# Kernel tuning notes

Measured on AMD Instinct MI355X. Metric: run time of the kernel, lower is better.

## Reference

```python
import jax, jax.numpy as jnp
import numpy as np

N = 50000
E = 800000
H = 8
DH = 32  # hidden 256 / heads 8


def gat_layer(h, src, dst, W, a_src, a_dst, b):
    # h: [N, 256] -> per-head projected features [N, H, DH]
    hp = (h @ W).reshape(N, H, DH)
    # per-node attention logits for src/dst roles: [N, H]
    s_src = jnp.einsum('nhd,hd->nh', hp, a_src)
    s_dst = jnp.einsum('nhd,hd->nh', hp, a_dst)
    e = jax.nn.leaky_relu(s_src[src] + s_dst[dst], negative_slope=0.2)  # [Et, H]
    # segment softmax over incoming edges of each dst node
    m = jax.ops.segment_max(e, dst, num_segments=N)  # [N, H]
    ex = jnp.exp(e - m[dst])
    denom = jax.ops.segment_sum(ex, dst, num_segments=N)  # [N, H] (>0: self-loops)
    alpha = ex / denom[dst]  # [Et, H]
    out = jax.ops.segment_sum(alpha[:, :, None] * hp[src], dst, num_segments=N)
    return out.reshape(N, H * DH) + b


def han_forward(x, edges, proj_W, proj_b, gat_W, gat_asrc, gat_adst, gat_b,
                sem_W1, sem_b1, sem_W2, cls_W1, cls_b1, cls_W2, cls_b2):
    h0 = x @ proj_W + proj_b  # [N, 256]
    loop = jnp.arange(N, dtype=edges.dtype)
    embs = []
    for p in range(edges.shape[0]):  # 3 meta-paths (fixed, small)
        src = jnp.concatenate([edges[p, 0], loop])  # add self-loops (PyG default)
        dst = jnp.concatenate([edges[p, 1], loop])
        h = h0
        for l in range(2):  # 2 GAT layers per meta-path
            h = gat_layer(h, src, dst, gat_W[p, l], gat_asrc[p, l], gat_adst[p, l], gat_b[p, l])
            h = jax.nn.elu(h)  # dropout: eval-mode no-op
        embs.append(h)
    emb = jnp.stack(embs, axis=1)  # [N, P, 256]
    scores = (jnp.tanh(emb @ sem_W1 + sem_b1) @ sem_W2).squeeze(-1)  # [N, P]
    w = jax.nn.softmax(scores, axis=1)
    z = jnp.sum(emb * w[:, :, None], axis=1)  # [N, 256]
    hcls = jax.nn.relu(z @ cls_W1 + cls_b1)
    logits = hcls @ cls_W2 + cls_b2  # [N, 2]
    return logits


def setup_inputs() -> dict:
    key = jax.random.key(0)
    ks = jax.random.split(key, 16)
    s = 0.05
    return {
        'x': jax.random.normal(ks[0], (N, 128), jnp.float32),
        'edges': jax.random.randint(ks[1], (3, 2, E), 0, N, dtype=jnp.int32),
        'proj_W': jax.random.normal(ks[2], (128, 256), jnp.float32) * s,
        'proj_b': jnp.zeros((256,), jnp.float32),
        'gat_W': jax.random.normal(ks[3], (3, 2, 256, 256), jnp.float32) * s,
        'gat_asrc': jax.random.normal(ks[4], (3, 2, H, DH), jnp.float32) * s,
        'gat_adst': jax.random.normal(ks[5], (3, 2, H, DH), jnp.float32) * s,
        'gat_b': jnp.zeros((3, 2, 256), jnp.float32),
        'sem_W1': jax.random.normal(ks[6], (256, 128), jnp.float32) * s,
        'sem_b1': jnp.zeros((128,), jnp.float32),
        'sem_W2': jax.random.normal(ks[7], (128, 1), jnp.float32) * s,
        'cls_W1': jax.random.normal(ks[8], (256, 128), jnp.float32) * s,
        'cls_b1': jnp.zeros((128,), jnp.float32),
        'cls_W2': jax.random.normal(ks[9], (128, 2), jnp.float32) * s,
        'cls_b2': jnp.zeros((2,), jnp.float32),
    }


def reference(x, edges, proj_W, proj_b, gat_W, gat_asrc, gat_adst, gat_b,
              sem_W1, sem_b1, sem_W2, cls_W1, cls_b1, cls_W2, cls_b2):
    return han_forward(x, edges, proj_W, proj_b, gat_W, gat_asrc, gat_adst, gat_b,
                       sem_W1, sem_b1, sem_W2, cls_W1, cls_b1, cls_W2, cls_b2)
```

## Files before the change

### kernel.cpp

```cpp
#include <hip/hip_runtime.h>
#include <hip/hip_fp16.h>
#include <math.h>

#define N_NODES 50000
#define N_EDG   800000
#define NH      8
#define DH      32
#define HID     256
#define MAXD    64
#define EPB     4096
#define PROJ_FB 88
#define PROJ_EB (176*EPB)
#define G3_FB   69
#define AGGB    12500

typedef __attribute__((ext_vector_type(8))) short bf16x8;
typedef __attribute__((ext_vector_type(4))) float f32x4;

#define GLL16(src, dst) __builtin_amdgcn_global_load_lds(                  \
    (const __attribute__((address_space(1))) void*)(const void*)(src),     \
    (__attribute__((address_space(3))) void*)(dst), 16, 0, 0)

__device__ __forceinline__ unsigned short f2bf(float x) {
    unsigned u = __float_as_uint(x);
    u += 0x7FFF + ((u >> 16) & 1);
    return (unsigned short)(u >> 16);
}
__device__ __forceinline__ float bf2f(unsigned short h) {
    return __uint_as_float(((unsigned)h) << 16);
}
__device__ __forceinline__ float fastrcp(float x) {
    float r;
    asm("v_rcp_f32 %0, %1" : "=v"(r) : "v"(x));
    return r;
}
__device__ __forceinline__ void split8(const float4& a, const float4& b,
                                       uint4& hi, uint4& lo) {
    float v[8] = {a.x,a.y,a.z,a.w,b.x,b.y,b.z,b.w};
    unsigned short h[8], l[8];
    #pragma unroll
    for (int i = 0; i < 8; ++i) { h[i] = f2bf(v[i]); l[i] = f2bf(v[i] - bf2f(h[i])); }
    hi = make_uint4(h[0]|((unsigned)h[1]<<16), h[2]|((unsigned)h[3]<<16),
                    h[4]|((unsigned)h[5]<<16), h[6]|((unsigned)h[7]<<16));
    lo = make_uint4(l[0]|((unsigned)l[1]<<16), l[2]|((unsigned)l[3]<<16),
                    l[4]|((unsigned)l[5]<<16), l[6]|((unsigned)l[7]<<16));
}
__device__ __forceinline__ void h8_to_pair(uint4 r, uint4& hi, uint4& lo) {
    const __half2* hp = (const __half2*)&r;
    unsigned short h[8], l[8];
    #pragma unroll
    for (int i = 0; i < 4; ++i) {
        float2 f = __half22float2(hp[i]);
        h[2*i]   = f2bf(f.x); l[2*i]   = f2bf(f.x - bf2f(h[2*i]));
        h[2*i+1] = f2bf(f.y); l[2*i+1] = f2bf(f.y - bf2f(h[2*i+1]));
    }
    hi = make_uint4(h[0]|((unsigned)h[1]<<16), h[2]|((unsigned)h[3]<<16),
                    h[4]|((unsigned)h[5]<<16), h[6]|((unsigned)h[7]<<16));
    lo = make_uint4(l[0]|((unsigned)l[1]<<16), l[2]|((unsigned)l[3]<<16),
                    l[4]|((unsigned)l[5]<<16), l[6]|((unsigned)l[7]<<16));
}

__device__ __forceinline__ void fmix2(float& alo, float& ahi, unsigned rv, float w) {
    asm("v_fma_mix_f32 %0, %1, %2, %0 op_sel:[0,0,0] op_sel_hi:[1,0,0]"
        : "+v"(alo) : "v"(rv), "v"(w));
    asm("v_fma_mix_f32 %0, %1, %2, %0 op_sel:[1,0,0] op_sel_hi:[1,0,0]"
        : "+v"(ahi) : "v"(rv), "v"(w));
}

__device__ __forceinline__ void fill_edges(const int* __restrict__ edges,
                                           int* __restrict__ cnt3,
                                           unsigned short* __restrict__ slots3,
                                           int fb, int ebase) {
    const int base = ebase + fb * EPB + (int)threadIdx.x;
    #pragma unroll 1
    for (int t = 0; t < 4; ++t) {
        int dd[4], ss[4];
        #pragma unroll
        for (int j = 0; j < 4; ++j) {
            int e = base + (t * 4 + j) * 256;
            if (e < 3 * N_EDG) {
                int p = e / N_EDG, i = e - p * N_EDG;
                const int* src = edges + (size_t)p * 2 * N_EDG;
                int s = src[i], d = src[N_EDG + i];
                ss[j] = min(max(s, 0), N_NODES - 1);
                dd[j] = p * N_NODES + min(max(d, 0), N_NODES - 1);
            } else { ss[j] = -1; dd[j] = 0; }
        }
        int pos[4];
        #pragma unroll
        for (int j = 0; j < 4; ++j)
            if (ss[j] >= 0) pos[j] = atomicAdd(&cnt3[dd[j]], 1);
        #pragma unroll
        for (int j = 0; j < 4; ++j)
            if (ss[j] >= 0 && pos[j] < MAXD)
                slots3[(size_t)dd[j] * MAXD + pos[j]] = (unsigned short)ss[j];
    }
}

__device__ __forceinline__ void agg_worker(
    int fb, int p, int l,
    const int* __restrict__ cnt3, const unsigned short* __restrict__ slots3,
    const float* __restrict__ ssrc3, const float* __restrict__ sdst3,
    const __half* __restrict__ hp3, const float* __restrict__ gatB,
    __half* __restrict__ emb16) {
    const int wid  = fb * 4 + ((int)threadIdx.x >> 6);
    const int lane = threadIdx.x & 63;
    if (wid >= N_NODES) return;
    const int n = wid;
    const unsigned short* srcs = slots3 + ((size_t)p * N_NODES + n) * MAXD;
    const float* s_src = ssrc3 + p * N_NODES * NH;
    const float* s_dst = sdst3 + p * N_NODES * NH;
    const __half* hp = hp3 + (size_t)p * N_NODES * HID;
    const float* bias = gatB + (2*p + l) * HID;
    const int deg = min(cnt3[p * N_NODES + n], MAXD);

    const int sub = lane & 31, eo = lane >> 5;
    const int h2  = sub >> 2;
    const float sd2 = s_dst[n*NH + h2];
    const uint4* hp4 = (const uint4*)hp;
    float dn = 0.f;
    float a0=0.f,a1=0.f,a2=0.f,a3=0.f,a4=0.f,a5=0.f,a6=0.f,a7=0.f;

    int i = eo;
    for (; i + 6 < deg; i += 8) {
        const int s0 = srcs[i];
        const int s1 = srcs[i + 2];
        const int s2 = srcs[i + 4];
        const int s3 = srcs[i + 6];
        const float x0 = s_src[s0*NH + h2];
        const float x1 = s_src[s1*NH + h2];
        const float x2 = s_src[s2*NH + h2];
        const float x3 = s_src[s3*NH + h2];
        const uint4 r0 = hp4[s0*32 + sub];
        const uint4 r1 = hp4[s1*32 + sub];
        const uint4 r2 = hp4[s2*32 + sub];
        const uint4 r3 = hp4[s3*32 + sub];
        float e0 = x0 + sd2; e0 = e0 > 0.f ? e0 : 0.2f * e0;
        float e1 = x1 + sd2; e1 = e1 > 0.f ? e1 : 0.2f * e1;
        float e2 = x2 + sd2; e2 = e2 > 0.f ? e2 : 0.2f * e2;
        float e3 = x3 + sd2; e3 = e3 > 0.f ? e3 : 0.2f * e3;
        const float w0 = __expf(e0), w1 = __expf(e1);
        const float w2 = __expf(e2), w3 = __expf(e3);
        dn += w0; dn += w1; dn += w2; dn += w3;
        fmix2(a0, a1, r0.x, w0); fmix2(a2, a3, r0.y, w0);
        fmix2(a4, a5, r0.z, w0); fmix2(a6, a7, r0.w, w0);
        fmix2(a0, a1, r1.x, w1); fmix2(a2, a3, r1.y, w1);
        fmix2(a4, a5, r1.z, w1); fmix2(a6, a7, r1.w, w1);
        fmix2(a0, a1, r2.x, w2); fmix2(a2, a3, r2.y, w2);
        fmix2(a4, a5, r2.z, w2); fmix2(a6, a7, r2.w, w2);
        fmix2(a0, a1, r3.x, w3); fmix2(a2, a3, r3.y, w3);
        fmix2(a4, a5, r3.z, w3); fmix2(a6, a7, r3.w, w3);
    }
    for (; i + 2 < deg; i += 4) {
        const int s0 = srcs[i];
        const int s1 = srcs[i + 2];
        const float x0 = s_src[s0*NH + h2];
        const float x1 = s_src[s1*NH + h2];
        const uint4 r0 = hp4[s0*32 + sub];
        const uint4 r1 = hp4[s1*32 + sub];
        float e0 = x0 + sd2; e0 = e0 > 0.f ? e0 : 0.2f * e0;
        float e1 = x1 + sd2; e1 = e1 > 0.f ? e1 : 0.2f * e1;
        const float w0 = __expf(e0), w1 = __expf(e1);
        dn += w0; dn += w1;
        fmix2(a0, a1, r0.x, w0); fmix2(a2, a3, r0.y, w0);
        fmix2(a4, a5, r0.z, w0); fmix2(a6, a7, r0.w, w0);
        fmix2(a0, a1, r1.x, w1); fmix2(a2, a3, r1.y, w1);
        fmix2(a4, a5, r1.z, w1); fmix2(a6, a7, r1.w, w1);
    }
    if (i < deg) {
        const int s0 = srcs[i];
        const float x0 = s_src[s0*NH + h2];
        const uint4 r0 = hp4[s0*32 + sub];
        float e0 = x0 + sd2; e0 = e0 > 0.f ? e0 : 0.2f * e0;
        const float w0 = __expf(e0);
        dn += w0;
        fmix2(a0, a1, r0.x, w0); fmix2(a2, a3, r0.y, w0);
        fmix2(a4, a5, r0.z, w0); fmix2(a6, a7, r0.w, w0);
    }
    dn += __shfl_xor(dn, 32);
    a0 += __shfl_xor(a0, 32); a1 += __shfl_xor(a1, 32);
    a2 += __shfl_xor(a2, 32); a3 += __shfl_xor(a3, 32);
    a4 += __shfl_xor(a4, 32); a5 += __shfl_xor(a5, 32);
    a6 += __shfl_xor(a6, 32); a7 += __shfl_xor(a7, 32);
    if (lane < 32) {
        float evs = s_src[n*NH + h2] + sd2;
        evs = evs > 0.f ? evs : 0.2f * evs;
        float ws = __expf(evs);
        dn += ws;
        const uint4 rs = hp4[n*32 + sub];
        fmix2(a0, a1, rs.x, ws); fmix2(a2, a3, rs.y, ws);
        fmix2(a4, a5, rs.z, ws); fmix2(a6, a7, rs.w, ws);

        float rdn = fastrcp(dn);
        float v[8] = {a0,a1,a2,a3,a4,a5,a6,a7};
        const float4 b0 = *(const float4*)&bias[sub*8];
        const float4 b1 = *(const float4*)&bias[sub*8 + 4];
        v[0]=v[0]*rdn+b0.x; v[1]=v[1]*rdn+b0.y; v[2]=v[2]*rdn+b0.z; v[3]=v[3]*rdn+b0.w;
        v[4]=v[4]*rdn+b1.x; v[5]=v[5]*rdn+b1.y; v[6]=v[6]*rdn+b1.z; v[7]=v[7]*rdn+b1.w;
        unsigned short hh[8];
        #pragma unroll
        for (int k = 0; k < 8; ++k) {
            float e = v[k] > 0.f ? v[k] : (__expf(v[k]) - 1.f);
            hh[k] = __half_as_ushort(__float2half(e));
        }
        size_t o = ((size_t)p * N_NODES + n) * HID + sub * 8;
        *(uint4*)&emb16[o] = make_uint4(hh[0]|((unsigned)hh[1]<<16), hh[2]|((unsigned)hh[3]<<16),
                                        hh[4]|((unsigned)hh[5]<<16), hh[6]|((unsigned)hh[7]<<16));
    }
}

__global__ __launch_bounds__(256)
void agg3y_k(const int* __restrict__ cnt3, const unsigned short* __restrict__ slots3,
             const float* __restrict__ ssrc3, const float* __restrict__ sdst3,
             const __half* __restrict__ hp3, const float* __restrict__ gatB,
             int l, __half* __restrict__ emb16) {
    agg_worker(blockIdx.x, blockIdx.y, l, cnt3, slots3, ssrc3, sdst3, hp3, gatB, emb16);
}

template<int NC, int ACT, int OUTMODE, int AMODE, int FILL>
__global__ __launch_bounds__(256)
void mfma_gemm_k(const float* __restrict__ A32p, const __half* __restrict__ A16p,
                 int lda,
                 const unsigned short* __restrict__ WThi,
                 const unsigned short* __restrict__ WTlo,
                 const float* __restrict__ bias,
                 float* __restrict__ C, __half* __restrict__ Ch,
                 int ldc, int M, int K,
                 const int* __restrict__ edges, int* __restrict__ cnt3,
                 unsigned short* __restrict__ slots3,
                 const float* __restrict__ w4z,
                 int aplanez, int cplanez) {
    __shared__ unsigned short sAh[128*32], sAl[128*32], sBh[128*32], sBl[128*32];
    const int gxk = (M + 127) >> 7;
    if constexpr (FILL) {
        if ((int)blockIdx.x >= gxk) {
            fill_edges(edges, cnt3, slots3,
                       ((int)blockIdx.x - gxk) + PROJ_FB * (int)blockIdx.y, 0);
            return;
        }
    }
    if (A16p) A16p += (size_t)blockIdx.z * aplanez;
    if (C)    C    += (size_t)blockIdx.z * cplanez;
    const int tid  = threadIdx.x;
    const int lane = tid & 63;
    const int w    = tid >> 6;
    const int wr   = w >> 1, wc = w & 1;
    const int r0   = blockIdx.x * 128;
    const int c0   = blockIdx.y * 128;
    const int l15  = lane & 15, q = lane >> 4;

    const int cl8   = (((lane & 3) ^ ((lane >> 4) & 3)) << 3);
    const int lrow  = w*32 + (lane >> 2);
    const int gbrow0 = c0 + lrow, gbrow1 = c0 + lrow + 16;
    const int lbase = w * 1024;

    const int srow = tid >> 2, slot = tid & 3;
    const int arow0 = min(r0 + srow,      M - 1);
    const int arow1 = min(r0 + srow + 64, M - 1);
    const size_t ga0 = (size_t)arow0 * lda + slot * 8;
    const size_t ga1 = (size_t)arow1 * lda + slot * 8;
    const int lda0 = srow*32 + ((slot ^ ((srow >> 2) & 3)) << 3);
    const int lda1 = lda0 + 64*32;

    float4 w0r, w1r;
    if constexpr (AMODE == 3) {
        w0r = *(const float4*)&w4z[arow0 * 4];
        w1r = *(const float4*)&w4z[arow1 * 4];
    }

    f32x4 acc[4][4];
    #pragma unroll
    for (int i = 0; i < 4; ++i)
        #pragma unroll
        for (int j = 0; j < 4; ++j) acc[i][j] = (f32x4){0.f, 0.f, 0.f, 0.f};

    const int swzF = (l15 >> 2) & 3;
    const int qs   = ((q ^ swzF) << 3);

    const int nsteps = K >> 5;
    for (int s = 0; s < nsteps; ++s) {
        const int kc = s << 5;
        __syncthreads();
        GLL16(&WThi[(size_t)gbrow0*K + kc + cl8], &sBh[lbase]);
        GLL16(&WThi[(size_t)gbrow1*K + kc + cl8], &sBh[lbase + 512]);
        GLL16(&WTlo[(size_t)gbrow0*K + kc + cl8], &sBl[lbase]);
        GLL16(&WTlo[(size_t)gbrow1*K + kc + cl8], &sBl[lbase + 512]);
        uint4 h0, l0, h1, l1;
        if constexpr (AMODE == 0) {
            float4 f0a = *(const float4*)&A32p[ga0 + kc];
            float4 f0b = *(const float4*)&A32p[ga0 + kc + 4];
            float4 f1a = *(const float4*)&A32p[ga1 + kc];
            float4 f1b = *(const float4*)&A32p[ga1 + kc + 4];
            split8(f0a, f0b, h0, l0);
            split8(f1a, f1b, h1, l1);
        } else if constexpr (AMODE == 1) {
            uint4 r0v = *(const uint4*)&A16p[ga0 + kc];
            uint4 r1v = *(const uint4*)&A16p[ga1 + kc];
            h8_to_pair(r0v, h0, l0);
            h8_to_pair(r1v, h1, l1);
        } else {
            const int off = kc + slot * 8;
            #pragma unroll
            for (int rr = 0; rr < 2; ++rr) {
                const int row = rr ? arow1 : arow0;
                const float4 wv = rr ? w1r : w0r;
                const __half2* e0 = (const __half2*)&A16p[(size_t)row * HID + off];
                const __half2* e1 = (const __half2*)&A16p[((size_t)N_NODES + row) * HID + off];
                const __half2* e2 = (const __half2*)&A16p[((size_t)2*N_NODES + row) * HID + off];
                float vv[8];
                #pragma unroll
                for (int j2 = 0; j2 < 4; ++j2) {
                    float2 fa = __half22float2(e0[j2]);
                    float2 fb2 = __half22float2(e1[j2]);
                    float2 fc = __half22float2(e2[j2]);
                    vv[2*j2]   = wv.x*fa.x + wv.y*fb2.x + wv.z*fc.x;
                    vv[2*j2+1] = wv.x*fa.y + wv.y*fb2.y + wv.z*fc.y;
                }
                if (rr) split8(*(const float4*)&vv[0], *(const float4*)&vv[4], h1, l1);
                else    split8(*(const float4*)&vv[0], *(const float4*)&vv[4], h0, l0);
            }
        }
        *(uint4*)&sAh[lda0] = h0; *(uint4*)&sAl[lda0] = l0;
        *(uint4*)&sAh[lda1] = h1; *(uint4*)&sAl[lda1] = l1;
        __syncthreads();

        bf16x8 fAh[4], fAl[4];
        #pragma unroll
        for (int t = 0; t < 4; ++t) {
            int ra = (wr*64 + t*16 + l15) * 32 + qs;
            fAh[t] = *(const bf16x8*)&sAh[ra];
            fAl[t] = *(const bf16x8*)&sAl[ra];
        }
        #pragma unroll
        for (int nt = 0; nt < 4; ++nt) {
            int rb = (wc*64 + nt*16 + l15) * 32 + qs;
            bf16x8 fBh = *(const bf16x8*)&sBh[rb];
            bf16x8 fBl = *(const bf16x8*)&sBl[rb];
            #pragma unroll
            for (int mt = 0; mt < 4; ++mt) {
                acc[mt][nt] = __builtin_amdgcn_mfma_f32_16x16x32_bf16(fAh[mt], fBh, acc[mt][nt], 0, 0, 0);
                acc[mt][nt] = __builtin_amdgcn_mfma_f32_16x16x32_bf16(fAh[mt], fBl, acc[mt][nt], 0, 0, 0);
                acc[mt][nt] = __builtin_amdgcn_mfma_f32_16x16x32_bf16(fAl[mt], fBh, acc[mt][nt], 0, 0, 0);
            }
        }
    }
    #pragma unroll
    for (int mt = 0; mt < 4; ++mt)
        #pragma unroll
        for (int nt = 0; nt < 4; ++nt) {
            int col = c0 + wc*64 + nt*16 + l15;
            float bb = bias ? bias[col] : 0.f;
            #pragma unroll
            for (int r = 0; r < 4; ++r) {
                int grow = r0 + wr*64 + mt*16 + q*4 + r;
                if (grow < M) {
                    float v = acc[mt][nt][r] + bb;
                    if (ACT == 1) {
                        float t = __expf(2.f * v);
                        v = 1.f - 2.f * fastrcp(1.f + t);
                    } else if (ACT == 2) v = fmaxf(v, 0.f);
                    size_t o = (size_t)grow * ldc + col;
                    if (OUTMODE == 2) Ch[o] = __float2half(v);
                    else              C[o] = v;
                }
            }
        }
}

template<int FILL>
__global__ __launch_bounds__(256)
void mfma_gemm3_k(const __half* __restrict__ A16p, int aoffz, int lda,
                  const unsigned short* __restrict__ WT, int l,
                  __half* __restrict__ hp3, int M,
                  const int* __restrict__ edges, int* __restrict__ cnt3,
                  unsigned short* __restrict__ slots3) {
    __shared__ unsigned short sAh[128*32], sAl[128*32], sBh[128*32], sBl[128*32];
    const int gx = (M + 127) >> 7;
    if constexpr (FILL) {
        if ((int)blockIdx.x >= gx) {
            fill_edges(edges, cnt3, slots3,
                       ((int)blockIdx.x - gx) + G3_FB * ((int)blockIdx.y + 2 * (int)blockIdx.z),
                       PROJ_EB);
            return;
        }
    }
    const int p = blockIdx.z;
    const __half* Ap = A16p + (size_t)p * aoffz;
    const unsigned short* WThi = WT + (size_t)(2*p + l) * 131072;
    const unsigned short* WTlo = WThi + 65536;
    __half* Ch = hp3 + (size_t)p * N_NODES * HID;
    const int K = HID;

    const int tid  = threadIdx.x;
    const int lane = tid & 63;
    const int w    = tid >> 6;
    const int wr   = w >> 1, wc = w & 1;
    const int r0   = blockIdx.x * 128;
    const int c0   = blockIdx.y * 128;
    const int l15  = lane & 15, q = lane >> 4;

    const int cl8   = (((lane & 3) ^ ((lane >> 4) & 3)) << 3);
    const int lrow  = w*32 + (lane >> 2);
    const int gbrow0 = c0 + lrow, gbrow1 = c0 + lrow + 16;
    const int lbase = w * 1024;

    const int srow = tid >> 2, slot = tid & 3;
    const size_t ga0 = (size_t)min(r0 + srow,      M - 1) * lda + slot * 8;
    const size_t ga1 = (size_t)min(r0 + srow + 64, M - 1) * lda + slot * 8;
    const int lda0 = srow*32 + ((slot ^ ((srow >> 2) & 3)) << 3);
    const int lda1 = lda0 + 64*32;

    f32x4 acc[4][4];
    #pragma unroll
    for (int i = 0; i < 4; ++i)
        #pragma unroll
        for (int j = 0; j < 4; ++j) acc[i][j] = (f32x4){0.f, 0.f, 0.f, 0.f};

    const int swzF = (l15 >> 2) & 3;
    const int qs   = ((q ^ swzF) << 3);

    for (int s = 0; s < 8; ++s) {
        const int kc = s << 5;
        __syncthreads();
        GLL16(&WThi[(size_t)gbrow0*K + kc + cl8], &sBh[lbase]);
        GLL16(&WThi[(size_t)gbrow1*K + kc + cl8], &sBh[lbase + 512]);
        GLL16(&WTlo[(size_t)gbrow0*K + kc + cl8], &sBl[lbase]);
        GLL16(&WTlo[(size_t)gbrow1*K + kc + cl8], &sBl[lbase + 512]);
        uint4 r0v = *(const uint4*)&Ap[ga0 + kc];
        uint4 r1v = *(const uint4*)&Ap[ga1 + kc];
        uint4 h0, l0, h1, l1;
        h8_to_pair(r0v, h0, l0);
        h8_to_pair(r1v, h1, l1);
        *(uint4*)&sAh[lda0] = h0; *(uint4*)&sAl[lda0] = l0;
        *(uint4*)&sAh[lda1] = h1; *(uint4*)&sAl[lda1] = l1;
        __syncthreads();

        bf16x8 fAh[4], fAl[4];
        #pragma unroll
        for (int t = 0; t < 4; ++t) {
            int ra = (wr*64 + t*16 + l15) * 32 + qs;
            fAh[t] = *(const bf16x8*)&sAh[ra];
            fAl[t] = *(const bf16x8*)&sAl[ra];
        }
        #pragma unroll
        for (int nt = 0; nt < 4; ++nt) {
            int rb = (wc*64 + nt*16 + l15) * 32 + qs;
            bf16x8 fBh = *(const bf16x8*)&sBh[rb];
            bf16x8 fBl = *(const bf16x8*)&sBl[rb];
            #pragma unroll
            for (int mt = 0; mt < 4; ++mt) {
                acc[mt][nt] = __builtin_amdgcn_mfma_f32_16x16x32_bf16(fAh[mt], fBh, acc[mt][nt], 0, 0, 0);
                acc[mt][nt] = __builtin_amdgcn_mfma_f32_16x16x32_bf16(fAh[mt], fBl, acc[mt][nt], 0, 0, 0);
                acc[mt][nt] = __builtin_amdgcn_mfma_f32_16x16x32_bf16(fAl[mt], fBh, acc[mt][nt], 0, 0, 0);
            }
        }
    }
    #pragma unroll
    for (int mt = 0; mt < 4; ++mt)
        #pragma unroll
        for (int nt = 0; nt < 4; ++nt) {
            int col = c0 + wc*64 + nt*16 + l15;
            #pragma unroll
            for (int r = 0; r < 4; ++r) {
                int grow = r0 + wr*64 + mt*16 + q*4 + r;
                if (grow < M)
                    Ch[(size_t)grow * HID + col] = __float2half(acc[mt][nt][r]);
            }
        }
}

__global__ __launch_bounds__(256)
void cvtWall_k(const float* __restrict__ gatW, const float* __restrict__ projW,
               const float* __restrict__ semW1, const float* __restrict__ clsW1,
               unsigned short* __restrict__ WT) {
    int y = blockIdx.y;
    const float* W; int K, N;
    if (y < 6)       { W = gatW + (size_t)y * 65536; K = 256; N = 256; }
    else if (y == 6) { W = projW; K = 128; N = 256; }
    else if (y == 7) { W = semW1; K = 256; N = 128; }
    else             { W = clsW1; K = 256; N = 128; }
    int idx = blockIdx.x * 256 + threadIdx.x;
    if (idx >= K * N) return;
    unsigned short* hi = WT + (size_t)y * 131072;
    unsigned short* lo = hi + 65536;
    int k = idx / N, n = idx - k * N;
    float v = W[idx];
    unsigned short h = f2bf(v);
    hi[n * K + k] = h;
    lo[n * K + k] = f2bf(v - bf2f(h));
}

__global__ __launch_bounds__(256)
void attn_scores3_k(const __half* __restrict__ hp3,
                    const float* __restrict__ gatAs, const float* __restrict__ gatAd,
                    int l, int pbase, float* __restrict__ ssrc3, float* __restrict__ sdst3) {
    int p = pbase + blockIdx.y;
    int gid = blockIdx.x * 256 + threadIdx.x;
    if (gid >= N_NODES * NH) return;
    int h = gid & 7;
    const __half2* hv = (const __half2*)(hp3 + (size_t)p * N_NODES * HID + (size_t)gid * DH);
    const float* a = gatAs + (2*p + l) * HID + h * DH;
    const float* d = gatAd + (2*p + l) * HID + h * DH;
    float ss = 0.f, sd = 0.f;
    #pragma unroll
    for (int j = 0; j < 8; ++j) {
        float4 av = ((const float4*)a)[j], dv = ((const float4*)d)[j];
        float2 f0 = __half22float2(hv[2*j]);
        float2 f1 = __half22float2(hv[2*j + 1]);
        ss += f0.x*av.x + f0.y*av.y + f1.x*av.z + f1.y*av.w;
        sd += f0.x*dv.x + f0.y*dv.y + f1.x*dv.z + f1.y*dv.w;
    }
    ssrc3[p * N_NODES * NH + gid] = ss;
    sdst3[p * N_NODES * NH + gid] = sd;
}

__global__ __launch_bounds__(256)
void zero_k(int* p, int n) { int i = blockIdx.x*256 + threadIdx.x; if (i < n) p[i] = 0; }

__global__ __launch_bounds__(256)
void score_w_k(const float* __restrict__ tb, const float* __restrict__ W2,
               float* __restrict__ w4) {
    int wid  = (blockIdx.x * blockDim.x + threadIdx.x) >> 6;
    int lane = threadIdx.x & 63;
    if (wid >= N_NODES) return;
    const int n = wid;
    float sc[3];
    #pragma unroll
    for (int p = 0; p < 3; ++p) {
        const float* tr = tb + (size_t)p * N_NODES * 128 + (size_t)n * 128;
        float part = tr[lane] * W2[lane] + tr[64 + lane] * W2[64 + lane];
        #pragma unroll
        for (int o = 1; o < 64; o <<= 1) part += __shfl_xor(part, o);
        sc[p] = part;
    }
    float m  = fmaxf(sc[0], fmaxf(sc[1], sc[2]));
    float e0 = __expf(sc[0]-m), e1 = __expf(sc[1]-m), e2 = __expf(sc[2]-m);
    float rs = fastrcp(e0 + e1 + e2);
    if (lane == 0)
        *(float4*)&w4[(size_t)n * 4] = make_float4(e0*rs, e1*rs, e2*rs, 0.f);
}

__global__ __launch_bounds__(256)
void logits_k(const float* __restrict__ hcls, const float* __restrict__ W2,
              const float* __restrict__ b2, float* __restrict__ out) {
    int gid = blockIdx.x*256 + threadIdx.x;
    if (gid >= N_NODES * 2) return;
    int n = gid >> 1, o = gid & 1;
    const float* hr = hcls + (size_t)n * 128;
    float a = b2[o];
    #pragma unroll 4
    for (int j = 0; j < 128; ++j) a += hr[j] * W2[j*2 + o];
    out[gid] = a;
}

extern "C" void kernel_launch(void* const* d_in, const int* in_sizes, int n_in,
                              void* d_out, int out_size, void* d_ws, size_t ws_size,
                              hipStream_t stream) {
    (void)in_sizes; (void)n_in; (void)out_size; (void)ws_size;
    const float* x     = (const float*)d_in[0];
    const int*   edges = (const int*)  d_in[1];
    const float* projW = (const float*)d_in[2];
    const float* projb = (const float*)d_in[3];
    const float* gatW  = (const float*)d_in[4];
    const float* gatAs = (const float*)d_in[5];
    const float* gatAd = (const float*)d_in[6];
    const float* gatB  = (const float*)d_in[7];
    const float* semW1 = (const float*)d_in[8];
    const float* semb1 = (const float*)d_in[9];
    const float* semW2 = (const float*)d_in[10];
    const float* clsW1 = (const float*)d_in[11];
    const float* clsb1 = (const float*)d_in[12];
    const float* clsW2 = (const float*)d_in[13];
    const float* clsb2 = (const float*)d_in[14];
    float* out = (float*)d_out;

    char* base = (char*)d_ws;
    const size_t PLANE = (size_t)N_NODES * HID * 2;
    __half* hp3   = (__half*)(base);
    __half* emb16 = (__half*)(base + 3*PLANE);
    __half* h016  = (__half*)(base + 6*PLANE);
    char* small = base + 7*PLANE;
    float* ssrc3 = (float*)small;
    float* sdst3 = ssrc3 + 3*(size_t)N_NODES*NH;
    int*   cnt3  = (int*)(sdst3 + 3*(size_t)N_NODES*NH);
    unsigned short* WT = (unsigned short*)(cnt3 + 3*N_NODES);
    unsigned short* slots3 = WT + 9*131072;
    float* w4 = (float*)(slots3 + (size_t)3*N_NODES*MAXD);
    float* t0 = (float*)(base);
    float* hcls = (float*)(base + 6*PLANE);

    dim3 blk(256);
    const int gx = (N_NODES + 127) / 128;

    cvtWall_k<<<dim3(256, 9), blk, 0, stream>>>(gatW, projW, semW1, clsW1, WT);
    zero_k  <<<(3*N_NODES+255)/256, blk, 0, stream>>>(cnt3, 3*N_NODES);

    mfma_gemm_k<256,0,2,0,1><<<dim3(gx + PROJ_FB, 2), blk, 0, stream>>>(
        x, nullptr, 128, WT + 6*131072, WT + 6*131072 + 65536, projb,
        nullptr, h016, 256, N_NODES, 128, edges, cnt3, slots3, nullptr, 0, 0);

    mfma_gemm3_k<1><<<dim3(gx + G3_FB, 2, 3), blk, 0, stream>>>(
        h016, 0, HID, WT, 0, hp3, N_NODES, edges, cnt3, slots3);

    attn_scores3_k<<<dim3((N_NODES*NH+255)/256, 3), blk, 0, stream>>>(
        hp3, gatAs, gatAd, 0, 0, ssrc3, sdst3);

    agg3y_k<<<dim3(AGGB, 3), blk, 0, stream>>>(
        cnt3, slots3, ssrc3, sdst3, hp3, gatB, 0, emb16);

    mfma_gemm3_k<0><<<dim3(gx, 2, 3), blk, 0, stream>>>(
        emb16, (int)((size_t)N_NODES*HID), HID, WT, 1, hp3, N_NODES,
        nullptr, nullptr, nullptr);

    attn_scores3_k<<<dim3((N_NODES*NH+255)/256, 3), blk, 0, stream>>>(
        hp3, gatAs, gatAd, 1, 0, ssrc3, sdst3);

    agg3y_k<<<dim3(AGGB, 3), blk, 0, stream>>>(
        cnt3, slots3, ssrc3, sdst3, hp3, gatB, 1, emb16);

    mfma_gemm_k<128,1,0,1,0><<<dim3(gx, 1, 3), blk, 0, stream>>>(
        nullptr, emb16, 256, WT + 7*131072, WT + 7*131072 + 65536, semb1,
        t0, nullptr, 128, N_NODES, 256, nullptr, nullptr, nullptr, nullptr,
        (int)((size_t)N_NODES*HID), N_NODES*128);

    score_w_k<<<dim3(AGGB), blk, 0, stream>>>(t0, semW2, w4);

    mfma_gemm_k<128,2,0,3,0><<<dim3(gx, 1), blk, 0, stream>>>(
        nullptr, emb16, HID, WT + 8*131072, WT + 8*131072 + 65536, clsb1,
        hcls, nullptr, 128, N_NODES, 256, nullptr, nullptr, nullptr, w4, 0, 0);

    logits_k<<<(N_NODES*2+255)/256, blk, 0, stream>>>(hcls, clsW2, clsb2, out);
}
```

Baseline: 968.1 us.

## Fuse classifier output layer into cls GEMM epilogue and use packed bf16 convert

The final 128->2 logits projection moves into the epilogue of the classifier GEMM. Each row's two outputs are reduced across lanes with shuffles and across the two column-warps through shared memory, so the hcls intermediate is no longer written and re-read and the separate logits kernel launch goes away. In the same change, the bf16 hi/lo splitting helpers switch from manual rounding to the packed v_cvt_pk_bf16_f32 instruction, which cuts ALU work wherever operands are split. The new epilogue adds shuffles and a barrier to the GEMM tail.

```diff
diff --git a/kernel.cpp b/kernel.cpp
--- a/kernel.cpp
+++ b/kernel.cpp
@@ -29,6 +29,11 @@
 __device__ __forceinline__ float bf2f(unsigned short h) {
     return __uint_as_float(((unsigned)h) << 16);
 }
+__device__ __forceinline__ unsigned cvtpk_bf16(float a, float b) {
+    unsigned r;
+    asm("v_cvt_pk_bf16_f32 %0, %1, %2" : "=v"(r) : "v"(a), "v"(b));
+    return r;
+}
 __device__ __forceinline__ float fastrcp(float x) {
     float r;
     asm("v_rcp_f32 %0, %1" : "=v"(r) : "v"(x));
@@ -36,28 +41,31 @@
 }
 __device__ __forceinline__ void split8(const float4& a, const float4& b,
                                        uint4& hi, uint4& lo) {
-    float v[8] = {a.x,a.y,a.z,a.w,b.x,b.y,b.z,b.w};
-    unsigned short h[8], l[8];
-    #pragma unroll
-    for (int i = 0; i < 8; ++i) { h[i] = f2bf(v[i]); l[i] = f2bf(v[i] - bf2f(h[i])); }
-    hi = make_uint4(h[0]|((unsigned)h[1]<<16), h[2]|((unsigned)h[3]<<16),
-                    h[4]|((unsigned)h[5]<<16), h[6]|((unsigned)h[7]<<16));
-    lo = make_uint4(l[0]|((unsigned)l[1]<<16), l[2]|((unsigned)l[3]<<16),
-                    l[4]|((unsigned)l[5]<<16), l[6]|((unsigned)l[7]<<16));
+    float f[8] = {a.x,a.y,a.z,a.w,b.x,b.y,b.z,b.w};
+    unsigned hpk[4], lpk[4];
+    #pragma unroll
+    for (int i = 0; i < 4; ++i) {
+        hpk[i] = cvtpk_bf16(f[2*i], f[2*i+1]);
+        float hl = __uint_as_float(hpk[i] << 16);
+        float hh = __uint_as_float(hpk[i] & 0xffff0000u);
+        lpk[i] = cvtpk_bf16(f[2*i] - hl, f[2*i+1] - hh);
+    }
+    hi = make_uint4(hpk[0], hpk[1], hpk[2], hpk[3]);
+    lo = make_uint4(lpk[0], lpk[1], lpk[2], lpk[3]);
 }
 __device__ __forceinline__ void h8_to_pair(uint4 r, uint4& hi, uint4& lo) {
     const __half2* hp = (const __half2*)&r;
-    unsigned short h[8], l[8];
+    unsigned hpk[4], lpk[4];
     #pragma unroll
     for (int i = 0; i < 4; ++i) {
         float2 f = __half22float2(hp[i]);
-        h[2*i]   = f2bf(f.x); l[2*i]   = f2bf(f.x - bf2f(h[2*i]));
-        h[2*i+1] = f2bf(f.y); l[2*i+1] = f2bf(f.y - bf2f(h[2*i+1]));
-    }
-    hi = make_uint4(h[0]|((unsigned)h[1]<<16), h[2]|((unsigned)h[3]<<16),
-                    h[4]|((unsigned)h[5]<<16), h[6]|((unsigned)h[7]<<16));
-    lo = make_uint4(l[0]|((unsigned)l[1]<<16), l[2]|((unsigned)l[3]<<16),
-                    l[4]|((unsigned)l[5]<<16), l[6]|((unsigned)l[7]<<16));
+        hpk[i] = cvtpk_bf16(f.x, f.y);
+        float hl = __uint_as_float(hpk[i] << 16);
+        float hh = __uint_as_float(hpk[i] & 0xffff0000u);
+        lpk[i] = cvtpk_bf16(f.x - hl, f.y - hh);
+    }
+    hi = make_uint4(hpk[0], hpk[1], hpk[2], hpk[3]);
+    lo = make_uint4(lpk[0], lpk[1], lpk[2], lpk[3]);
 }
 
 __device__ __forceinline__ void fmix2(float& alo, float& ahi, unsigned rv, float w) {
@@ -229,7 +237,8 @@
                  const int* __restrict__ edges, int* __restrict__ cnt3,
                  unsigned short* __restrict__ slots3,
                  const float* __restrict__ w4z,
-                 int aplanez, int cplanez) {
+                 int aplanez, int cplanez,
+                 const float* __restrict__ logW2, const float* __restrict__ logB2) {
     __shared__ unsigned short sAh[128*32], sAl[128*32], sBh[128*32], sBl[128*32];
     const int gxk = (M + 127) >> 7;
     if constexpr (FILL) {
@@ -344,6 +353,56 @@
             }
         }
     }
+    if constexpr (OUTMODE == 3) {
+        __syncthreads();
+        float* red = (float*)sAh;
+        float pl[16][2];
+        #pragma unroll
+        for (int mt = 0; mt < 4; ++mt)
+            #pragma unroll
+            for (int r = 0; r < 4; ++r) {
+                float p0 = 0.f, p1 = 0.f;
+                #pragma unroll
+                for (int nt = 0; nt < 4; ++nt) {
+                    int col = wc*64 + nt*16 + l15;
+                    float v = fmaxf(acc[mt][nt][r] + bias[col], 0.f);
+                    p0 += v * logW2[col*2];
+                    p1 += v * logW2[col*2 + 1];
+                }
+                #pragma unroll
+                for (int o = 1; o < 16; o <<= 1) {
+                    p0 += __shfl_xor(p0, o);
+                    p1 += __shfl_xor(p1, o);
+                }
+                pl[mt*4 + r][0] = p0;
+                pl[mt*4 + r][1] = p1;
+            }
+        if (wc == 1 && l15 == 0) {
+            #pragma unroll
+            for (int mt = 0; mt < 4; ++mt)
+                #pragma unroll
+                for (int r = 0; r < 4; ++r) {
+                    int rl = wr*64 + mt*16 + q*4 + r;
+                    red[rl*2]     = pl[mt*4 + r][0];
+                    red[rl*2 + 1] = pl[mt*4 + r][1];
+                }
+        }
+        __syncthreads();
+        if (wc == 0 && l15 == 0) {
+            #pragma unroll
+            for (int mt = 0; mt < 4; ++mt)
+                #pragma unroll
+                for (int r = 0; r < 4; ++r) {
+                    int rl = wr*64 + mt*16 + q*4 + r;
+                    int grow = r0 + rl;
+                    if (grow < M) {
+                        C[(size_t)grow*2]     = pl[mt*4+r][0] + red[rl*2]     + logB2[0];
+                        C[(size_t)grow*2 + 1] = pl[mt*4+r][1] + red[rl*2 + 1] + logB2[1];
+                    }
+                }
+        }
+        return;
+    }
     #pragma unroll
     for (int mt = 0; mt < 4; ++mt)
         #pragma unroll
@@ -538,19 +597,6 @@
     float rs = fastrcp(e0 + e1 + e2);
     if (lane == 0)
         *(float4*)&w4[(size_t)n * 4] = make_float4(e0*rs, e1*rs, e2*rs, 0.f);
-}
-
-__global__ __launch_bounds__(256)
-void logits_k(const float* __restrict__ hcls, const float* __restrict__ W2,
-              const float* __restrict__ b2, float* __restrict__ out) {
-    int gid = blockIdx.x*256 + threadIdx.x;
-    if (gid >= N_NODES * 2) return;
-    int n = gid >> 1, o = gid & 1;
-    const float* hr = hcls + (size_t)n * 128;
-    float a = b2[o];
-    #pragma unroll 4
-    for (int j = 0; j < 128; ++j) a += hr[j] * W2[j*2 + o];
-    out[gid] = a;
 }
 
 extern "C" void kernel_launch(void* const* d_in, const int* in_sizes, int n_in,
@@ -587,7 +633,6 @@
     unsigned short* slots3 = WT + 9*131072;
     float* w4 = (float*)(slots3 + (size_t)3*N_NODES*MAXD);
     float* t0 = (float*)(base);
-    float* hcls = (float*)(base + 6*PLANE);
 
     dim3 blk(256);
     const int gx = (N_NODES + 127) / 128;
@@ -597,7 +642,8 @@
 
     mfma_gemm_k<256,0,2,0,1><<<dim3(gx + PROJ_FB, 2), blk, 0, stream>>>(
         x, nullptr, 128, WT + 6*131072, WT + 6*131072 + 65536, projb,
-        nullptr, h016, 256, N_NODES, 128, edges, cnt3, slots3, nullptr, 0, 0);
+        nullptr, h016, 256, N_NODES, 128, edges, cnt3, slots3, nullptr, 0, 0,
+        nullptr, nullptr);
 
     mfma_gemm3_k<1><<<dim3(gx + G3_FB, 2, 3), blk, 0, stream>>>(
         h016, 0, HID, WT, 0, hp3, N_NODES, edges, cnt3, slots3);
@@ -621,13 +667,12 @@
     mfma_gemm_k<128,1,0,1,0><<<dim3(gx, 1, 3), blk, 0, stream>>>(
         nullptr, emb16, 256, WT + 7*131072, WT + 7*131072 + 65536, semb1,
         t0, nullptr, 128, N_NODES, 256, nullptr, nullptr, nullptr, nullptr,
-        (int)((size_t)N_NODES*HID), N_NODES*128);
+        (int)((size_t)N_NODES*HID), N_NODES*128, nullptr, nullptr);
 
     score_w_k<<<dim3(AGGB), blk, 0, stream>>>(t0, semW2, w4);
 
-    mfma_gemm_k<128,2,0,3,0><<<dim3(gx, 1), blk, 0, stream>>>(
+    mfma_gemm_k<128,2,3,3,0><<<dim3(gx, 1), blk, 0, stream>>>(
         nullptr, emb16, HID, WT + 8*131072, WT + 8*131072 + 65536, clsb1,
-        hcls, nullptr, 128, N_NODES, 256, nullptr, nullptr, nullptr, w4, 0, 0);
-
-    logits_k<<<(N_NODES*2+255)/256, blk, 0, stream>>>(hcls, clsW2, clsb2, out);
-}
+        out, nullptr, 0, N_NODES, 256, nullptr, nullptr, nullptr, w4, 0, 0,
+        clsW2, clsb2);
+}
```

Result: faster. 942.3 us (-2.7%).
